# Performance work log

Measured on AMD Instinct MI355X. Metric: run time of the kernel, lower is better.

## Reference

```python
import jax, jax.numpy as jnp
import numpy as np

B, S, D = 16, 2048, 128
NEG = -1000000000.0


def setup_inputs() -> dict:
    key = jax.random.key(0)
    kq, kk, kv = jax.random.split(key, 3)
    q = jax.random.normal(kq, (B, S, D), dtype=jnp.float32)
    k = jax.random.normal(kk, (B, S, D), dtype=jnp.float32)
    v = jax.random.normal(kv, (B, S, D), dtype=jnp.float32)
    # causal mask: True entries are masked out (filled with -1e9)
    mask = jnp.broadcast_to(
        jnp.triu(jnp.ones((S, S), dtype=bool), k=1)[None, :, :], (B, S, S)
    )
    return {"q": q, "k": k, "v": v, "mask": mask}


def reference(q, k, v, mask):
    # attn = q @ k^T / sqrt(d_k), masked_fill, softmax over keys, attn @ v
    scale = jnp.sqrt(jnp.asarray(D, dtype=q.dtype))
    attn = jnp.einsum("bqd,bkd->bqk", q, k) / scale
    attn = jnp.where(mask, jnp.asarray(NEG, dtype=attn.dtype), attn)
    attn = jax.nn.softmax(attn, axis=2)
    out = jnp.einsum("bqk,bkd->bqd", attn, v)
    return (out, attn)
```

## Files before the change

kernel.cpp:

```cpp
#include <hip/hip_runtime.h>

#define B_ 16
#define S_ 2048
#define D_ 128

typedef __attribute__((ext_vector_type(8))) short bf16x8;
typedef __attribute__((ext_vector_type(4))) float f32x4;
typedef __attribute__((ext_vector_type(2))) unsigned int u32x2;
typedef __attribute__((ext_vector_type(4))) unsigned int u32x4;

__device__ __forceinline__ unsigned short f2bf(float f) {
    unsigned int u = __builtin_bit_cast(unsigned int, f);
    u += 0x7fff + ((u >> 16) & 1);
    return (unsigned short)(u >> 16);
}

__device__ __forceinline__ void gload16(const void* g, void* l) {
    __builtin_amdgcn_global_load_lds(
        (const __attribute__((address_space(1))) void*)g,
        (__attribute__((address_space(3))) void*)l, 16, 0, 0);
}

#define WAITV(n) asm volatile("s_waitcnt vmcnt(" #n ")" ::: "memory")

__global__ __launch_bounds__(256, 4)
void conv_kv(const float* __restrict__ kg, const float* __restrict__ vg,
             char* __restrict__ kws, char* __restrict__ vws)
{
    __shared__ float lt[64 * 132];
    const int bid = blockIdx.x;
    if (bid < 512) {
        const float* src = kg + ((long)bid << 13);
        char* dst = kws + ((long)bid << 14);
#pragma unroll
        for (int it = 0; it < 4; ++it) {
            const int c = threadIdx.x + it * 256;
            const int r = c >> 4, j = c & 15;
            f32x4 a = *(const f32x4*)(src + r * 128 + j * 8);
            f32x4 cc = *(const f32x4*)(src + r * 128 + j * 8 + 4);
            u32x4 p;
            p[0] = (unsigned)f2bf(a[0]) | ((unsigned)f2bf(a[1]) << 16);
            p[1] = (unsigned)f2bf(a[2]) | ((unsigned)f2bf(a[3]) << 16);
            p[2] = (unsigned)f2bf(cc[0]) | ((unsigned)f2bf(cc[1]) << 16);
            p[3] = (unsigned)f2bf(cc[2]) | ((unsigned)f2bf(cc[3]) << 16);
            *(u32x4*)(dst + r * 256 + ((j ^ (r & 7)) << 4)) = p;
        }
    } else {
        const int vb = bid - 512;
        const float* src = vg + ((long)vb << 13);
        char* dst = vws + ((long)vb << 14);
#pragma unroll
        for (int it = 0; it < 8; ++it) {
            const int c = threadIdx.x + it * 256;
            const int r = c >> 5, q = c & 31;
            *(f32x4*)(lt + r * 132 + q * 4) = *(const f32x4*)(src + r * 128 + q * 4);
        }
        __syncthreads();
#pragma unroll
        for (int it = 0; it < 4; ++it) {
            const int c = threadIdx.x + it * 256;
            const int d = c >> 3, jc = c & 7;
            unsigned short e[8];
#pragma unroll
            for (int ee = 0; ee < 8; ++ee) e[ee] = f2bf(lt[(jc * 8 + ee) * 132 + d]);
            u32x4 p;
            p[0] = (unsigned)e[0] | ((unsigned)e[1] << 16);
            p[1] = (unsigned)e[2] | ((unsigned)e[3] << 16);
            p[2] = (unsigned)e[4] | ((unsigned)e[5] << 16);
            p[3] = (unsigned)e[6] | ((unsigned)e[7] << 16);
            *(u32x4*)(dst + d * 128 + ((jc ^ (d & 7)) << 4)) = p;
        }
    }
}

__device__ __forceinline__ int qtile_of(int b, int t) {
    const int f = (t & 1) ? (t >> 1) : (31 - (t >> 1));
    return (b & 8) ? (31 - f) : f;
}

__global__ __launch_bounds__(256, 4)
void sumexp(const float* __restrict__ qg, const char* __restrict__ kws,
            float* __restrict__ lg, float* __restrict__ attng)
{
    __shared__ char kT[2][16384];

    const int tid = threadIdx.x, lane = tid & 63, w = tid >> 6;
    const int l15 = lane & 15, l4 = lane >> 4;
    const int bid = blockIdx.x;
    const int b = bid >> 5;
    const int qt = qtile_of(b, bid & 31);
    const int q0 = qt * 64;
    const float scale = 0.088388347648318447f;

    bf16x8 qf[4];
    {
        const float* qrow = qg + ((long)b * S_ + q0 + w * 16 + l15) * D_;
#pragma unroll
        for (int kk = 0; kk < 4; ++kk) {
            const int d0 = kk * 32 + l4 * 8;
            f32x4 a = *(const f32x4*)(qrow + d0);
            f32x4 c = *(const f32x4*)(qrow + d0 + 4);
            bf16x8 tt;
            tt[0] = (short)f2bf(a[0]); tt[1] = (short)f2bf(a[1]);
            tt[2] = (short)f2bf(a[2]); tt[3] = (short)f2bf(a[3]);
            tt[4] = (short)f2bf(c[0]); tt[5] = (short)f2bf(c[1]);
            tt[6] = (short)f2bf(c[2]); tt[7] = (short)f2bf(c[3]);
            qf[kk] = tt;
        }
    }
    WAITV(0);

    float sum[4] = {0.f, 0.f, 0.f, 0.f};
    const char* kb0 = kws + ((long)(b * 32) << 14);

#pragma unroll
    for (int it = 0; it < 4; ++it)
        gload16(kb0 + (w * 4 + it) * 1024 + lane * 16, &kT[0][(w * 4 + it) * 1024]);

    int buf = 0;
    for (int kt = 0; kt <= qt; ++kt) {
        const bool pf = (kt < qt);
        if (pf) {
            const char* kn = kb0 + ((long)(kt + 1) << 14);
#pragma unroll
            for (int it = 0; it < 4; ++it)
                gload16(kn + (w * 4 + it) * 1024 + lane * 16, &kT[buf ^ 1][(w * 4 + it) * 1024]);
            WAITV(4);
        } else {
            WAITV(0);
        }
        __builtin_amdgcn_s_barrier();
        __builtin_amdgcn_sched_barrier(0);

        f32x4 acc[4];
        __builtin_amdgcn_s_setprio(1);
#pragma unroll
        for (int n = 0; n < 4; ++n) {
            f32x4 a = {0.f, 0.f, 0.f, 0.f};
            const int krow = n * 16 + l15;
            const int rb = krow * 256;
            const int swz = (krow & 7) << 4;
#pragma unroll
            for (int kk = 0; kk < 4; ++kk) {
                bf16x8 bf = *(const bf16x8*)(&kT[buf][rb + ((l4 * 16 + kk * 64) ^ swz)]);
                a = __builtin_amdgcn_mfma_f32_16x16x32_bf16(qf[kk], bf, a, 0, 0, 0);
            }
            acc[n] = a;
        }
        __builtin_amdgcn_s_setprio(0);

        const bool diag = (kt == qt);
#pragma unroll
        for (int n = 0; n < 4; ++n)
#pragma unroll
            for (int r = 0; r < 4; ++r) {
                if (!(diag && (n * 16 + l15 > w * 16 + l4 * 4 + r)))
                    sum[r] += __expf(acc[n][r] * scale);
            }
        __builtin_amdgcn_sched_barrier(0);
        __builtin_amdgcn_s_barrier();
        buf ^= 1;
    }

#pragma unroll
    for (int off = 1; off < 16; off <<= 1)
#pragma unroll
        for (int r = 0; r < 4; ++r)
            sum[r] += __shfl_xor(sum[r], off, 64);
    if (l15 == 0) {
#pragma unroll
        for (int r = 0; r < 4; ++r)
            lg[(long)b * S_ + q0 + w * 16 + l4 * 4 + r] = 1.f / sum[r];
    }

    float* attn_base = attng + ((long)b * S_ + q0) * S_;
    const int col0 = (qt + 1) * 64;
    if (col0 < S_) {
        const int nch = (S_ - col0) >> 2;
        const f32x4 z = {0.f, 0.f, 0.f, 0.f};
        for (int row = w; row < 64; row += 4) {
            float* rbase = attn_base + (long)row * S_ + col0;
            for (int c = lane; c < nch; c += 64)
                *(f32x4*)(rbase + c * 4) = z;
        }
    }
}

__global__ __launch_bounds__(256, 2)
void attn_pv(const float* __restrict__ qg, const char* __restrict__ kws,
             const char* __restrict__ vws, const float* __restrict__ lg,
             float* __restrict__ outg, float* __restrict__ attng)
{
    __shared__ char kT[2][16384];
    __shared__ char vT[2][16384];
    __shared__ unsigned short pT[4][16 * 64];

    const int tid = threadIdx.x, lane = tid & 63, w = tid >> 6;
    const int l15 = lane & 15, l4 = lane >> 4;
    const int bid = blockIdx.x;
    const int b = bid >> 5;
    const int qt = qtile_of(b, bid & 31);
    const int q0 = qt * 64;
    const float scale = 0.088388347648318447f;

    bf16x8 qf[4];
    {
        const float* qrow = qg + ((long)b * S_ + q0 + w * 16 + l15) * D_;
#pragma unroll
        for (int kk = 0; kk < 4; ++kk) {
            const int d0 = kk * 32 + l4 * 8;
            f32x4 a = *(const f32x4*)(qrow + d0);
            f32x4 c = *(const f32x4*)(qrow + d0 + 4);
            bf16x8 tt;
            tt[0] = (short)f2bf(a[0]); tt[1] = (short)f2bf(a[1]);
            tt[2] = (short)f2bf(a[2]); tt[3] = (short)f2bf(a[3]);
            tt[4] = (short)f2bf(c[0]); tt[5] = (short)f2bf(c[1]);
            tt[6] = (short)f2bf(c[2]); tt[7] = (short)f2bf(c[3]);
            qf[kk] = tt;
        }
    }
    float invl[4];
#pragma unroll
    for (int r = 0; r < 4; ++r)
        invl[r] = lg[(long)b * S_ + q0 + w * 16 + l4 * 4 + r];
    WAITV(0);

    f32x4 oacc[8];
#pragma unroll
    for (int n = 0; n < 8; ++n) oacc[n] = (f32x4){0.f, 0.f, 0.f, 0.f};

    const char* kb0 = kws + ((long)(b * 32) << 14);
    const char* vb0 = vws + ((long)(b * 32) << 14);
    float* attn_base = attng + ((long)b * S_ + q0) * S_;

#pragma unroll
    for (int it = 0; it < 4; ++it)
        gload16(kb0 + (w * 4 + it) * 1024 + lane * 16, &kT[0][(w * 4 + it) * 1024]);
#pragma unroll
    for (int it = 0; it < 4; ++it)
        gload16(vb0 + (w * 4 + it) * 1024 + lane * 16, &vT[0][(w * 4 + it) * 1024]);

    int buf = 0;
    for (int kt = 0; kt <= qt; ++kt) {
        const bool pf = (kt < qt);
        if (pf) {
            const char* kn = kb0 + ((long)(kt + 1) << 14);
            const char* vn = vb0 + ((long)(kt + 1) << 14);
#pragma unroll
            for (int it = 0; it < 4; ++it)
                gload16(kn + (w * 4 + it) * 1024 + lane * 16, &kT[buf ^ 1][(w * 4 + it) * 1024]);
#pragma unroll
            for (int it = 0; it < 4; ++it)
                gload16(vn + (w * 4 + it) * 1024 + lane * 16, &vT[buf ^ 1][(w * 4 + it) * 1024]);
        }
        if (kt == 0) { if (pf) { WAITV(8); } else { WAITV(0); } }
        else         { if (pf) { WAITV(24); } else { WAITV(16); } }
        __builtin_amdgcn_s_barrier();
        __builtin_amdgcn_sched_barrier(0);

        f32x4 acc[4];
        __builtin_amdgcn_s_setprio(1);
#pragma unroll
        for (int n = 0; n < 4; ++n) {
            f32x4 a = {0.f, 0.f, 0.f, 0.f};
            const int krow = n * 16 + l15;
            const int rb = krow * 256;
            const int swz = (krow & 7) << 4;
#pragma unroll
            for (int kk = 0; kk < 4; ++kk) {
                bf16x8 bf = *(const bf16x8*)(&kT[buf][rb + ((l4 * 16 + kk * 64) ^ swz)]);
                a = __builtin_amdgcn_mfma_f32_16x16x32_bf16(qf[kk], bf, a, 0, 0, 0);
            }
            acc[n] = a;
        }
        __builtin_amdgcn_s_setprio(0);

        const bool diag = (kt == qt);
        float* abase = attn_base + (long)(w * 16) * S_ + kt * 64;
#pragma unroll
        for (int n = 0; n < 4; ++n)
#pragma unroll
            for (int r = 0; r < 4; ++r) {
                float p;
                if (diag && (n * 16 + l15 > w * 16 + l4 * 4 + r)) p = 0.f;
                else p = __expf(acc[n][r] * scale);
                abase[(long)(l4 * 4 + r) * S_ + n * 16 + l15] = p * invl[r];
                const int prow = l4 * 4 + r;
                *(unsigned short*)((char*)&pT[w][0] + prow * 128 +
                                   ((n * 32 + l15 * 2) ^ ((prow & 7) << 4))) = f2bf(p);
            }
        asm volatile("s_waitcnt lgkmcnt(0)" ::: "memory");
        __builtin_amdgcn_sched_barrier(0);

        bf16x8 pa[2];
#pragma unroll
        for (int kk = 0; kk < 2; ++kk)
            pa[kk] = *(const bf16x8*)((const char*)&pT[w][0] + l15 * 128 +
                                      ((l4 * 16 + kk * 64) ^ ((l15 & 7) << 4)));
        __builtin_amdgcn_s_setprio(1);
#pragma unroll
        for (int n = 0; n < 8; ++n) {
            const int vrow = n * 16 + l15;
            const int rb2 = vrow * 128;
            const int swz2 = (vrow & 7) << 4;
#pragma unroll
            for (int kk = 0; kk < 2; ++kk) {
                bf16x8 bv = *(const bf16x8*)(&vT[buf][rb2 + ((l4 * 16 + kk * 64) ^ swz2)]);
                oacc[n] = __builtin_amdgcn_mfma_f32_16x16x32_bf16(pa[kk], bv, oacc[n], 0, 0, 0);
            }
        }
        __builtin_amdgcn_s_setprio(0);
        __builtin_amdgcn_sched_barrier(0);
        __builtin_amdgcn_s_barrier();
        buf ^= 1;
    }

    float* obase = outg + ((long)b * S_ + q0 + w * 16) * D_;
#pragma unroll
    for (int n = 0; n < 8; ++n)
#pragma unroll
        for (int r = 0; r < 4; ++r)
            obase[(long)(l4 * 4 + r) * D_ + n * 16 + l15] = oacc[n][r] * invl[r];
}

__global__ __launch_bounds__(256, 2)
void attn_fallback(const float* __restrict__ qg, const float* __restrict__ kg,
                   const float* __restrict__ vg,
                   float* __restrict__ outg, float* __restrict__ attng)
{
    __shared__ unsigned short kT[64 * 128];
    __shared__ unsigned short vT[128 * 64];
    __shared__ unsigned short pT[4][16 * 64];
    const int tid = threadIdx.x, lane = tid & 63, w = tid >> 6;
    const int l15 = lane & 15, l4 = lane >> 4;
    const int bid = blockIdx.x;
    const int b = bid >> 5, qt = 31 - (bid & 31), q0 = qt * 64;
    const float scale = 0.088388347648318447f;
    bf16x8 qf[4];
    {
        const float* qrow = qg + ((long)b * S_ + q0 + w * 16 + l15) * D_;
#pragma unroll
        for (int kk = 0; kk < 4; ++kk) {
            const int d0 = kk * 32 + l4 * 8;
            f32x4 a = *(const f32x4*)(qrow + d0);
            f32x4 c = *(const f32x4*)(qrow + d0 + 4);
            bf16x8 t;
            t[0] = (short)f2bf(a[0]); t[1] = (short)f2bf(a[1]);
            t[2] = (short)f2bf(a[2]); t[3] = (short)f2bf(a[3]);
            t[4] = (short)f2bf(c[0]); t[5] = (short)f2bf(c[1]);
            t[6] = (short)f2bf(c[2]); t[7] = (short)f2bf(c[3]);
            qf[kk] = t;
        }
    }
    float m[4], l[4];
#pragma unroll
    for (int r = 0; r < 4; ++r) { m[r] = -1e30f; l[r] = 0.f; }
    for (int kt = 0; kt <= qt; ++kt) {
        __syncthreads();
        {
            const float* kbase = kg + ((long)b * S_ + kt * 64) * D_;
#pragma unroll
            for (int it = 0; it < 8; ++it) {
                const int c = tid + it * 256, row = c >> 5, dc = c & 31;
                f32x4 a = *(const f32x4*)(kbase + row * D_ + dc * 4);
                u32x2 p;
                p[0] = (unsigned)f2bf(a[0]) | ((unsigned)f2bf(a[1]) << 16);
                p[1] = (unsigned)f2bf(a[2]) | ((unsigned)f2bf(a[3]) << 16);
                *(u32x2*)((char*)kT + row * 256 + ((dc * 8) ^ ((row & 7) << 4))) = p;
            }
        }
        __syncthreads();
        f32x4 acc[4];
#pragma unroll
        for (int n = 0; n < 4; ++n) {
            f32x4 a = {0.f, 0.f, 0.f, 0.f};
            const int krow = n * 16 + l15, rb = krow * 256, swz = (krow & 7) << 4;
#pragma unroll
            for (int kk = 0; kk < 4; ++kk) {
                bf16x8 bf = *(const bf16x8*)((const char*)kT + rb + ((l4 * 16 + kk * 64) ^ swz));
                a = __builtin_amdgcn_mfma_f32_16x16x32_bf16(qf[kk], bf, a, 0, 0, 0);
            }
            acc[n] = a;
        }
        const bool diag = (kt == qt);
        float tm[4] = {-3e38f, -3e38f, -3e38f, -3e38f};
#pragma unroll
        for (int n = 0; n < 4; ++n)
#pragma unroll
            for (int r = 0; r < 4; ++r) {
                float s = acc[n][r] * scale;
                if (diag && (n * 16 + l15 > w * 16 + l4 * 4 + r)) s = -3e38f;
                acc[n][r] = s; tm[r] = fmaxf(tm[r], s);
            }
#pragma unroll
        for (int off = 1; off < 16; off <<= 1)
#pragma unroll
            for (int r = 0; r < 4; ++r) tm[r] = fmaxf(tm[r], __shfl_xor(tm[r], off, 64));
        float sum[4], mn[4];
#pragma unroll
        for (int r = 0; r < 4; ++r) {
            mn[r] = fmaxf(m[r], tm[r]);
            float s0 = 0.f;
#pragma unroll
            for (int n = 0; n < 4; ++n) s0 += __expf(acc[n][r] - mn[r]);
            sum[r] = s0;
        }
#pragma unroll
        for (int off = 1; off < 16; off <<= 1)
#pragma unroll
            for (int r = 0; r < 4; ++r) sum[r] += __shfl_xor(sum[r], off, 64);
#pragma unroll
        for (int r = 0; r < 4; ++r) { l[r] = l[r] * __expf(m[r] - mn[r]) + sum[r]; m[r] = mn[r]; }
    }
    float invl[4];
#pragma unroll
    for (int r = 0; r < 4; ++r) invl[r] = 1.f / l[r];
    f32x4 oacc[8];
#pragma unroll
    for (int n = 0; n < 8; ++n) oacc[n] = (f32x4){0.f, 0.f, 0.f, 0.f};
    float* attn_base = attng + ((long)b * S_ + q0) * S_;
    for (int kt = 0; kt <= qt; ++kt) {
        __syncthreads();
        {
            const float* kbase = kg + ((long)b * S_ + kt * 64) * D_;
#pragma unroll
            for (int it = 0; it < 8; ++it) {
                const int c = tid + it * 256, row = c >> 5, dc = c & 31;
                f32x4 a = *(const f32x4*)(kbase + row * D_ + dc * 4);
                u32x2 p;
                p[0] = (unsigned)f2bf(a[0]) | ((unsigned)f2bf(a[1]) << 16);
                p[1] = (unsigned)f2bf(a[2]) | ((unsigned)f2bf(a[3]) << 16);
                *(u32x2*)((char*)kT + row * 256 + ((dc * 8) ^ ((row & 7) << 4))) = p;
            }
        }
        {
            const float* vbase = vg + ((long)b * S_ + kt * 64) * D_;
#pragma unroll
            for (int it = 0; it < 8; ++it) {
                const int c = tid + it * 256, kr = c & 63, dq = c >> 6;
                f32x4 a = *(const f32x4*)(vbase + kr * D_ + dq * 4);
#pragma unroll
                for (int j = 0; j < 4; ++j) {
                    const int d = dq * 4 + j;
                    *(unsigned short*)((char*)vT + d * 128 + ((kr * 2) ^ ((d & 7) << 4))) = f2bf(a[j]);
                }
            }
        }
        __syncthreads();
        f32x4 acc[4];
#pragma unroll
        for (int n = 0; n < 4; ++n) {
            f32x4 a = {0.f, 0.f, 0.f, 0.f};
            const int krow = n * 16 + l15, rb = krow * 256, swz = (krow & 7) << 4;
#pragma unroll
            for (int kk = 0; kk < 4; ++kk) {
                bf16x8 bf = *(const bf16x8*)((const char*)kT + rb + ((l4 * 16 + kk * 64) ^ swz));
                a = __builtin_amdgcn_mfma_f32_16x16x32_bf16(qf[kk], bf, a, 0, 0, 0);
            }
            acc[n] = a;
        }
        const bool diag = (kt == qt);
#pragma unroll
        for (int n = 0; n < 4; ++n)
#pragma unroll
            for (int r = 0; r < 4; ++r) {
                float s = acc[n][r] * scale;
                if (diag && (n * 16 + l15 > w * 16 + l4 * 4 + r)) s = -3e38f;
                const float p = __expf(s - m[r]) * invl[r];
                attn_base[(long)(w * 16 + l4 * 4 + r) * S_ + kt * 64 + n * 16 + l15] = p;
                const int prow = l4 * 4 + r;
                *(unsigned short*)((char*)&pT[w][0] + prow * 128 + ((n * 32 + l15 * 2) ^ ((prow & 7) << 4))) = f2bf(p);
            }
        asm volatile("s_waitcnt lgkmcnt(0)" ::: "memory");
        __builtin_amdgcn_sched_barrier(0);
        bf16x8 pa[2];
#pragma unroll
        for (int kk = 0; kk < 2; ++kk)
            pa[kk] = *(const bf16x8*)((const char*)&pT[w][0] + l15 * 128 + ((l4 * 16 + kk * 64) ^ ((l15 & 7) << 4)));
#pragma unroll
        for (int n = 0; n < 8; ++n) {
            const int vrow = n * 16 + l15, rb = vrow * 128, swz = (vrow & 7) << 4;
#pragma unroll
            for (int kk = 0; kk < 2; ++kk) {
                bf16x8 bv = *(const bf16x8*)((const char*)vT + rb + ((l4 * 16 + kk * 64) ^ swz));
                oacc[n] = __builtin_amdgcn_mfma_f32_16x16x32_bf16(pa[kk], bv, oacc[n], 0, 0, 0);
            }
        }
    }
    {
        float* obase = outg + ((long)b * S_ + q0 + w * 16) * D_;
#pragma unroll
        for (int n = 0; n < 8; ++n)
#pragma unroll
            for (int r = 0; r < 4; ++r)
                obase[(long)(l4 * 4 + r) * D_ + n * 16 + l15] = oacc[n][r];
    }
    {
        const int col0 = (qt + 1) * 64;
        if (col0 < S_) {
            const int nch = (S_ - col0) >> 2;
            const f32x4 z = {0.f, 0.f, 0.f, 0.f};
            for (int row = w; row < 64; row += 4) {
                float* rbase = attn_base + (long)row * S_ + col0;
                for (int c = lane; c < nch; c += 64)
                    *(f32x4*)(rbase + c * 4) = z;
            }
        }
    }
}

extern "C" void kernel_launch(void* const* d_in, const int* in_sizes, int n_in,
                              void* d_out, int out_size, void* d_ws, size_t ws_size,
                              hipStream_t stream) {
    const float* q = (const float*)d_in[0];
    const float* k = (const float*)d_in[1];
    const float* v = (const float*)d_in[2];
    float* out  = (float*)d_out;
    float* attn = out + (long)B_ * S_ * D_;
    const size_t NEED = 131072 + 2u * 8388608u;
    if (ws_size >= NEED) {
        float* lg = (float*)d_ws;
        char* kws = (char*)d_ws + 131072;
        char* vws = kws + 8388608;
        conv_kv<<<dim3(1024), dim3(256), 0, stream>>>(k, v, kws, vws);
        sumexp<<<dim3(512), dim3(256), 0, stream>>>(q, kws, lg, attn);
        attn_pv<<<dim3(512), dim3(256), 0, stream>>>(q, kws, vws, lg, out, attn);
    } else {
        attn_fallback<<<dim3(512), dim3(256), 0, stream>>>(q, k, v, out, attn);
    }
}
```

Measured before the change: 126.9 us.

## Rework attn_pv to 32x32 MFMA with 2x2 wave split and register-shuffled P

The PV kernel switches from 16x16x32 to 32x32x16 bf16 MFMAs, splitting the four waves into a 2x2 grid over query rows and key columns. The S^T product leaves P in registers, so it is rearranged with cross-half lane shuffles instead of a round trip through LDS. Attention probabilities are now written as 16-byte vector stores along each row instead of scattered scalar stores. Each wave now holds only half the key columns, so the two partial output accumulators are summed through LDS at the end, adding a reduction pass and two block barriers.

```diff
diff --git a/kernel.cpp b/kernel.cpp
--- a/kernel.cpp
+++ b/kernel.cpp
@@ -6,6 +6,7 @@
 
 typedef __attribute__((ext_vector_type(8))) short bf16x8;
 typedef __attribute__((ext_vector_type(4))) float f32x4;
+typedef __attribute__((ext_vector_type(16))) float f32x16;
 typedef __attribute__((ext_vector_type(2))) unsigned int u32x2;
 typedef __attribute__((ext_vector_type(4))) unsigned int u32x4;
 
@@ -191,122 +192,140 @@
              const char* __restrict__ vws, const float* __restrict__ lg,
              float* __restrict__ outg, float* __restrict__ attng)
 {
-    __shared__ char kT[2][16384];
-    __shared__ char vT[2][16384];
-    __shared__ unsigned short pT[4][16 * 64];
+    __shared__ char lds[65536];
 
     const int tid = threadIdx.x, lane = tid & 63, w = tid >> 6;
-    const int l15 = lane & 15, l4 = lane >> 4;
+    const int wq = w >> 1, wk = w & 1;
+    const int l31 = lane & 31, hi = lane >> 5;
     const int bid = blockIdx.x;
     const int b = bid >> 5;
-    const int qt = qtile_of(b, bid & 31);
-    const int q0 = qt * 64;
+    const int qti = qtile_of(b, bid & 31);
+    const int q0 = qti * 64;
+    const int nt = qti + 1;
     const float scale = 0.088388347648318447f;
-
-    bf16x8 qf[4];
+    const int qrow = q0 + wq * 32 + l31;
+
+    bf16x8 qf[8];
     {
-        const float* qrow = qg + ((long)b * S_ + q0 + w * 16 + l15) * D_;
-#pragma unroll
-        for (int kk = 0; kk < 4; ++kk) {
-            const int d0 = kk * 32 + l4 * 8;
-            f32x4 a = *(const f32x4*)(qrow + d0);
-            f32x4 c = *(const f32x4*)(qrow + d0 + 4);
-            bf16x8 tt;
-            tt[0] = (short)f2bf(a[0]); tt[1] = (short)f2bf(a[1]);
-            tt[2] = (short)f2bf(a[2]); tt[3] = (short)f2bf(a[3]);
-            tt[4] = (short)f2bf(c[0]); tt[5] = (short)f2bf(c[1]);
-            tt[6] = (short)f2bf(c[2]); tt[7] = (short)f2bf(c[3]);
-            qf[kk] = tt;
-        }
-    }
-    float invl[4];
-#pragma unroll
-    for (int r = 0; r < 4; ++r)
-        invl[r] = lg[(long)b * S_ + q0 + w * 16 + l4 * 4 + r];
+        const float* qr = qg + ((long)b * S_ + qrow) * D_;
+#pragma unroll
+        for (int km = 0; km < 8; ++km) {
+            const int d0 = km * 16 + hi * 8;
+            f32x4 a = *(const f32x4*)(qr + d0);
+            f32x4 c = *(const f32x4*)(qr + d0 + 4);
+            bf16x8 t;
+            t[0] = (short)f2bf(a[0]); t[1] = (short)f2bf(a[1]);
+            t[2] = (short)f2bf(a[2]); t[3] = (short)f2bf(a[3]);
+            t[4] = (short)f2bf(c[0]); t[5] = (short)f2bf(c[1]);
+            t[6] = (short)f2bf(c[2]); t[7] = (short)f2bf(c[3]);
+            qf[km] = t;
+        }
+    }
+    const float invl_l = lg[(long)b * S_ + qrow];
     WAITV(0);
 
-    f32x4 oacc[8];
-#pragma unroll
-    for (int n = 0; n < 8; ++n) oacc[n] = (f32x4){0.f, 0.f, 0.f, 0.f};
+    f32x16 oacc[4];
+#pragma unroll
+    for (int dt = 0; dt < 4; ++dt)
+#pragma unroll
+        for (int i = 0; i < 16; ++i) oacc[dt][i] = 0.f;
 
     const char* kb0 = kws + ((long)(b * 32) << 14);
     const char* vb0 = vws + ((long)(b * 32) << 14);
-    float* attn_base = attng + ((long)b * S_ + q0) * S_;
 
 #pragma unroll
     for (int it = 0; it < 4; ++it)
-        gload16(kb0 + (w * 4 + it) * 1024 + lane * 16, &kT[0][(w * 4 + it) * 1024]);
+        gload16(kb0 + it * 4096 + tid * 16, lds + it * 4096 + tid * 16);
 #pragma unroll
     for (int it = 0; it < 4; ++it)
-        gload16(vb0 + (w * 4 + it) * 1024 + lane * 16, &vT[0][(w * 4 + it) * 1024]);
+        gload16(vb0 + it * 4096 + tid * 16, lds + 32768 + it * 4096 + tid * 16);
+
+    const int krow = wk * 32 + l31;
+    const int krb = krow * 256;
+    const int ksw = krow & 7;
 
     int buf = 0;
-    for (int kt = 0; kt <= qt; ++kt) {
-        const bool pf = (kt < qt);
+    for (int kt = 0; kt < nt; ++kt) {
+        const bool pf = (kt + 1 < nt);
         if (pf) {
             const char* kn = kb0 + ((long)(kt + 1) << 14);
             const char* vn = vb0 + ((long)(kt + 1) << 14);
+            const int db = (buf ^ 1) * 16384;
 #pragma unroll
             for (int it = 0; it < 4; ++it)
-                gload16(kn + (w * 4 + it) * 1024 + lane * 16, &kT[buf ^ 1][(w * 4 + it) * 1024]);
+                gload16(kn + it * 4096 + tid * 16, lds + db + it * 4096 + tid * 16);
 #pragma unroll
             for (int it = 0; it < 4; ++it)
-                gload16(vn + (w * 4 + it) * 1024 + lane * 16, &vT[buf ^ 1][(w * 4 + it) * 1024]);
+                gload16(vn + it * 4096 + tid * 16, lds + 32768 + db + it * 4096 + tid * 16);
         }
         if (kt == 0) { if (pf) { WAITV(8); } else { WAITV(0); } }
-        else         { if (pf) { WAITV(24); } else { WAITV(16); } }
+        else         { if (pf) { WAITV(12); } else { WAITV(4); } }
         __builtin_amdgcn_s_barrier();
         __builtin_amdgcn_sched_barrier(0);
 
-        f32x4 acc[4];
+        const char* kbuf = lds + buf * 16384;
+        const char* vbuf = lds + 32768 + buf * 16384;
+
+        f32x16 acc;
+#pragma unroll
+        for (int i = 0; i < 16; ++i) acc[i] = 0.f;
         __builtin_amdgcn_s_setprio(1);
 #pragma unroll
-        for (int n = 0; n < 4; ++n) {
-            f32x4 a = {0.f, 0.f, 0.f, 0.f};
-            const int krow = n * 16 + l15;
-            const int rb = krow * 256;
-            const int swz = (krow & 7) << 4;
-#pragma unroll
-            for (int kk = 0; kk < 4; ++kk) {
-                bf16x8 bf = *(const bf16x8*)(&kT[buf][rb + ((l4 * 16 + kk * 64) ^ swz)]);
-                a = __builtin_amdgcn_mfma_f32_16x16x32_bf16(qf[kk], bf, a, 0, 0, 0);
-            }
-            acc[n] = a;
+        for (int km = 0; km < 8; ++km) {
+            bf16x8 kf = *(const bf16x8*)(kbuf + krb + (((km * 2 + hi) ^ ksw) << 4));
+            acc = __builtin_amdgcn_mfma_f32_32x32x16_bf16(kf, qf[km], acc, 0, 0, 0);
         }
         __builtin_amdgcn_s_setprio(0);
 
-        const bool diag = (kt == qt);
-        float* abase = attn_base + (long)(w * 16) * S_ + kt * 64;
-#pragma unroll
-        for (int n = 0; n < 4; ++n)
-#pragma unroll
-            for (int r = 0; r < 4; ++r) {
-                float p;
-                if (diag && (n * 16 + l15 > w * 16 + l4 * 4 + r)) p = 0.f;
-                else p = __expf(acc[n][r] * scale);
-                abase[(long)(l4 * 4 + r) * S_ + n * 16 + l15] = p * invl[r];
-                const int prow = l4 * 4 + r;
-                *(unsigned short*)((char*)&pT[w][0] + prow * 128 +
-                                   ((n * 32 + l15 * 2) ^ ((prow & 7) << 4))) = f2bf(p);
-            }
-        asm volatile("s_waitcnt lgkmcnt(0)" ::: "memory");
-        __builtin_amdgcn_sched_barrier(0);
+        const int kbase = kt * 64 + wk * 32;
+        float p[16];
+#pragma unroll
+        for (int r = 0; r < 16; ++r) {
+            const int kl = (r & 3) + 8 * (r >> 2) + 4 * hi;
+            p[r] = (kbase + kl > qrow) ? 0.f : __expf(acc[r] * scale);
+        }
+        unsigned W[8], PW[8];
+#pragma unroll
+        for (int i = 0; i < 8; ++i)
+            W[i] = (unsigned)f2bf(p[2 * i]) | ((unsigned)f2bf(p[2 * i + 1]) << 16);
+#pragma unroll
+        for (int i = 0; i < 8; ++i)
+            PW[i] = (unsigned)__shfl_xor((int)W[i], 32, 64);
 
         bf16x8 pa[2];
-#pragma unroll
-        for (int kk = 0; kk < 2; ++kk)
-            pa[kk] = *(const bf16x8*)((const char*)&pT[w][0] + l15 * 128 +
-                                      ((l4 * 16 + kk * 64) ^ ((l15 & 7) << 4)));
+        float* arow = attng + ((long)b * S_ + qrow) * S_ + kbase;
+#pragma unroll
+        for (int kc = 0; kc < 2; ++kc) {
+            u32x4 fr;
+            fr[0] = hi ? PW[kc * 4 + 2] : W[kc * 4 + 0];
+            fr[1] = hi ? PW[kc * 4 + 3] : W[kc * 4 + 1];
+            fr[2] = hi ? W[kc * 4 + 2] : PW[kc * 4 + 0];
+            fr[3] = hi ? W[kc * 4 + 3] : PW[kc * 4 + 1];
+            pa[kc] = __builtin_bit_cast(bf16x8, fr);
+            f32x4 s0, s1;
+            s0[0] = __builtin_bit_cast(float, fr[0] << 16) * invl_l;
+            s0[1] = __builtin_bit_cast(float, fr[0] & 0xffff0000u) * invl_l;
+            s0[2] = __builtin_bit_cast(float, fr[1] << 16) * invl_l;
+            s0[3] = __builtin_bit_cast(float, fr[1] & 0xffff0000u) * invl_l;
+            s1[0] = __builtin_bit_cast(float, fr[2] << 16) * invl_l;
+            s1[1] = __builtin_bit_cast(float, fr[2] & 0xffff0000u) * invl_l;
+            s1[2] = __builtin_bit_cast(float, fr[3] << 16) * invl_l;
+            s1[3] = __builtin_bit_cast(float, fr[3] & 0xffff0000u) * invl_l;
+            *(f32x4*)(arow + kc * 16 + hi * 8) = s0;
+            *(f32x4*)(arow + kc * 16 + hi * 8 + 4) = s1;
+        }
+
         __builtin_amdgcn_s_setprio(1);
 #pragma unroll
-        for (int n = 0; n < 8; ++n) {
-            const int vrow = n * 16 + l15;
-            const int rb2 = vrow * 128;
-            const int swz2 = (vrow & 7) << 4;
-#pragma unroll
-            for (int kk = 0; kk < 2; ++kk) {
-                bf16x8 bv = *(const bf16x8*)(&vT[buf][rb2 + ((l4 * 16 + kk * 64) ^ swz2)]);
-                oacc[n] = __builtin_amdgcn_mfma_f32_16x16x32_bf16(pa[kk], bv, oacc[n], 0, 0, 0);
+        for (int dt = 0; dt < 4; ++dt) {
+            const int d = dt * 32 + l31;
+            const int rowb = d * 128;
+            const int sw = (d & 7) << 4;
+#pragma unroll
+            for (int kc = 0; kc < 2; ++kc) {
+                const int jc = wk * 4 + kc * 2 + hi;
+                bf16x8 vf = *(const bf16x8*)(vbuf + rowb + ((jc << 4) ^ sw));
+                oacc[dt] = __builtin_amdgcn_mfma_f32_32x32x16_bf16(pa[kc], vf, oacc[dt], 0, 0, 0);
             }
         }
         __builtin_amdgcn_s_setprio(0);
@@ -315,12 +334,35 @@
         buf ^= 1;
     }
 
-    float* obase = outg + ((long)b * S_ + q0 + w * 16) * D_;
-#pragma unroll
-    for (int n = 0; n < 8; ++n)
-#pragma unroll
-        for (int r = 0; r < 4; ++r)
-            obase[(long)(l4 * 4 + r) * D_ + n * 16 + l15] = oacc[n][r] * invl[r];
+    __syncthreads();
+    float* red = (float*)lds;
+    if (wk) {
+#pragma unroll
+        for (int dt = 0; dt < 4; ++dt)
+#pragma unroll
+            for (int r = 0; r < 16; ++r) {
+                const int qr = (r & 3) + 8 * (r >> 2) + 4 * hi;
+                red[wq * 4096 + qr * 128 + dt * 32 + l31] = oacc[dt][r];
+            }
+    }
+    __syncthreads();
+    if (!wk) {
+        float iv[16];
+#pragma unroll
+        for (int r = 0; r < 16; ++r) {
+            const int qr = (r & 3) + 8 * (r >> 2) + 4 * hi;
+            iv[r] = __shfl(invl_l, qr, 64);
+        }
+        float* ob = outg + ((long)b * S_ + q0 + wq * 32) * D_;
+#pragma unroll
+        for (int dt = 0; dt < 4; ++dt)
+#pragma unroll
+            for (int r = 0; r < 16; ++r) {
+                const int qr = (r & 3) + 8 * (r >> 2) + 4 * hi;
+                ob[(long)qr * D_ + dt * 32 + l31] =
+                    (oacc[dt][r] + red[wq * 4096 + qr * 128 + dt * 32 + l31]) * iv[r];
+            }
+    }
 }
 
 __global__ __launch_bounds__(256, 2)
```

Measured after the change: 120.3 us. -5.2%, faster.
